# Performance work log

Measured on AMD Instinct MI355X. Metric: run time of the kernel, lower is better.

## Reference

```python
import jax, jax.numpy as jnp
import numpy as np

N_TOKENS = 8192
TOP_K = 2
N_EXPERTS = 8
D_IN = 2048
D_OUT = 2048


def setup_inputs() -> dict:
    key = jax.random.key(0)
    k1, k2, k3, k4 = jax.random.split(key, 4)
    inputs = jax.random.normal(k1, (N_TOKENS, D_IN), dtype=jnp.float32)
    # stored as [E, out, in], matching nn.Parameter(torch.empty(E, output_size, input_size))
    expert_weights = 0.02 * jax.random.normal(k2, (N_EXPERTS, D_OUT, D_IN), dtype=jnp.float32)
    gates = jax.nn.softmax(jax.random.normal(k3, (N_TOKENS, TOP_K), dtype=jnp.float32), axis=-1)
    # per (token, slot) expert assignment, then sort by expert as the router would
    flat_experts = jax.random.randint(k4, (N_TOKENS * TOP_K,), 0, N_EXPERTS, dtype=jnp.int32)
    sorted_scattered_idxs = jnp.argsort(flat_experts).astype(jnp.int32)
    sorted_expert_idxs = flat_experts[sorted_scattered_idxs]
    expert_offsets = jnp.cumsum(jnp.bincount(flat_experts, length=N_EXPERTS)).astype(jnp.int32)
    return {
        "inputs": inputs,
        "expert_weights": expert_weights,
        "gates": gates,
        "k": TOP_K,
        "sorted_expert_idxs": sorted_expert_idxs,
        "sorted_scattered_idxs": sorted_scattered_idxs,
        "expert_offsets": expert_offsets,
    }


def reference(inputs, expert_weights, gates, k, sorted_expert_idxs, sorted_scattered_idxs, expert_offsets):
    N, d_in = inputs.shape
    E = expert_weights.shape[0]
    Nk = N * k
    # forward permutes weight [E, out, in] -> [E, in, out]
    W = jnp.transpose(expert_weights, (0, 2, 1))
    d_out = W.shape[-1]
    # invert the sort: expert id for each flat (token, slot) index
    expert_per_flat = jnp.zeros((Nk,), dtype=sorted_expert_idxs.dtype).at[
        sorted_scattered_idxs].set(sorted_expert_idxs)
    # scatter2scatter: out_flat[j] = x[j // k] @ W[expert_per_flat[j]]
    x_rep = jnp.repeat(inputs, k, axis=0)  # [N*k, d_in]
    out_flat = jnp.zeros((Nk, d_out), dtype=inputs.dtype)
    for e in range(E):  # small fixed expert count; masked grouped GEMM
        mask = (expert_per_flat == e)[:, None]
        out_flat = out_flat + jnp.where(mask, x_rep, 0.0) @ W[e]
    # combine: (gates.unsqueeze(1) @ output_expanded).squeeze(1)
    out = jnp.einsum('nk,nkd->nd', gates, out_flat.reshape(N, k, d_out))
    return out
```

## Files before the change

kernel.cpp:

```cpp
#include <hip/hip_runtime.h>
#include <hip/hip_bf16.h>
#include <stdint.h>

#define NTOK   8192
#define TOPK   2
#define NEXP   8
#define DIN    2048
#define DOUT   2048
#define NK     (NTOK*TOPK)

#define BM 256
#define BN 128
#define BK 32
#define KTILES  (DIN/BK)
#define SLOT    24576
#define NBUF    3

typedef __bf16 bf16_8 __attribute__((ext_vector_type(8)));
typedef float  f32x4  __attribute__((ext_vector_type(4)));

__device__ __forceinline__ void gl2lds16(const void* g, void* l) {
  auto gp = reinterpret_cast<const __attribute__((address_space(1))) uint32_t*>(
      reinterpret_cast<uintptr_t>(g));
  auto lp = reinterpret_cast<__attribute__((address_space(3))) uint32_t*>(
      reinterpret_cast<uintptr_t>(l));
  __builtin_amdgcn_global_load_lds(gp, lp, 16, 0, 0);
}

__global__ void cvt_all(const float4* __restrict__ w, uint4* __restrict__ wD,
                        const float4* __restrict__ x, uint4* __restrict__ xD,
                        int nW) {
  int b = blockIdx.x;
  const float4* src;
  uint4* dst;
  int i;
  if (b < nW) { src = w; dst = wD; i = b * 256 + threadIdx.x; }
  else        { src = x; dst = xD; i = (b - nW) * 256 + threadIdx.x; }
  float4 a0 = src[2 * i];
  float4 a1 = src[2 * i + 1];
  union { __bf16 h[8]; uint4 u; } r;
  r.h[0] = (__bf16)a0.x; r.h[1] = (__bf16)a0.y; r.h[2] = (__bf16)a0.z; r.h[3] = (__bf16)a0.w;
  r.h[4] = (__bf16)a1.x; r.h[5] = (__bf16)a1.y; r.h[6] = (__bf16)a1.z; r.h[7] = (__bf16)a1.w;
  dst[i] = r.u;
}

__global__ __launch_bounds__(512, 4)
void moe_gemm(const __bf16* __restrict__ X,
              const __bf16* __restrict__ W,
              const int* __restrict__ ssi,
              const int* __restrict__ offs,
              __bf16* __restrict__ flat)
{
  __shared__ char lds[NBUF * SLOT];
  __shared__ int  sTok[BM];
  __shared__ int  sF[BM];

  const int tid = threadIdx.x;
  const int bid = blockIdx.x;
  const int nt  = bid & 15;
  const int mtg = bid >> 4;

  int start = 0, end = 0, e, cum = 0, prev = 0, mloc = 0, found = 0;
  for (e = 0; e < NEXP; ++e) {
    int oe  = offs[e];
    int seg = oe - prev;
    int t   = (seg + BM - 1) >> 8;
    if (mtg < cum + t) { start = prev; end = oe; mloc = mtg - cum; found = 1; break; }
    cum += t; prev = oe;
  }
  if (!found) return;

  const int m0 = start + mloc * BM;

  if (tid < BM) {
    int p     = m0 + tid;
    int valid = p < end;
    int f     = ssi[valid ? p : (end - 1)];
    sTok[tid] = f >> 1;
    sF[tid]   = valid ? f : -1;
  }
  __syncthreads();

  const int rs = tid >> 2;
  const int kc = (tid & 3) ^ ((tid >> 3) & 3);
  const __bf16* pA0 = X + (size_t)sTok[rs]       * DIN + kc * 8;
  const __bf16* pA1 = X + (size_t)sTok[rs + 128] * DIN + kc * 8;
  const __bf16* wBp = W + (size_t)e * DOUT * DIN + (size_t)(nt * BN) * DIN;
  const __bf16* pB0 = wBp + (size_t)rs * DIN + kc * 8;
  char* wsl = (char*)lds + (tid >> 6) * 1024;

  gl2lds16(pA0, wsl);           gl2lds16(pA1, wsl + 8192);
  gl2lds16(pB0, wsl + 16384);
  pA0 += BK; pA1 += BK; pB0 += BK;
  gl2lds16(pA0, wsl + SLOT);    gl2lds16(pA1, wsl + SLOT + 8192);
  gl2lds16(pB0, wsl + SLOT + 16384);
  pA0 += BK; pA1 += BK; pB0 += BK;

  const int w   = tid >> 6;
  const int l   = tid & 63;
  const int wm  = w >> 1, wn = w & 1;
  const int lr  = l & 15;
  const int kq  = l >> 4;
  const int kqs = kq ^ ((lr >> 1) & 3);
  const char* aBase = (const char*)lds + (wm * 64 + lr) * 64 + kqs * 16;
  const char* bBase = (const char*)lds + 16384 + (wn * 64 + lr) * 64 + kqs * 16;

  asm volatile("s_waitcnt vmcnt(3)" ::: "memory");
  __builtin_amdgcn_s_barrier();

  f32x4 acc[4][4] = {};
  int rOff = 0;
  int sOff = 2 * SLOT;

  for (int t = 0; t < KTILES; ++t) {
    if (t < KTILES - 2) {
      char* d = wsl + sOff;
      gl2lds16(pA0, d);  gl2lds16(pA1, d + 8192);  gl2lds16(pB0, d + 16384);
      pA0 += BK; pA1 += BK; pB0 += BK;
      sOff = (sOff == (NBUF - 1) * SLOT) ? 0 : sOff + SLOT;
    }

    const char* aB = aBase + rOff;
    const char* bB = bBase + rOff;
    rOff = (rOff == (NBUF - 1) * SLOT) ? 0 : rOff + SLOT;

    bf16_8 af[4], bf[4];
#pragma unroll
    for (int i = 0; i < 4; ++i) af[i] = *(const bf16_8*)(aB + i * 1024);
#pragma unroll
    for (int i = 0; i < 4; ++i) bf[i] = *(const bf16_8*)(bB + i * 1024);

#pragma unroll
    for (int am = 0; am < 4; ++am)
#pragma unroll
      for (int bn = 0; bn < 4; ++bn)
        acc[am][bn] = __builtin_amdgcn_mfma_f32_16x16x32_bf16(
            af[am], bf[bn], acc[am][bn], 0, 0, 0);

    if (t < KTILES - 2)       { asm volatile("s_waitcnt vmcnt(3)" ::: "memory"); }
    else if (t == KTILES - 2) { asm volatile("s_waitcnt vmcnt(0)" ::: "memory"); }
    if (t < KTILES - 1) __builtin_amdgcn_s_barrier();
  }

  const int colBase = nt * BN + wn * 64 + lr;
  const int rq = kq * 4;
#pragma unroll
  for (int am = 0; am < 4; ++am) {
#pragma unroll
    for (int v = 0; v < 4; ++v) {
      int rl = wm * 64 + am * 16 + rq + v;
      int f  = sF[rl];
      if (f < 0) continue;
      __bf16* row = flat + (size_t)f * DOUT + colBase;
#pragma unroll
      for (int bn = 0; bn < 4; ++bn)
        row[bn * 16] = (__bf16)acc[am][bn][v];
    }
  }
}

__global__ __launch_bounds__(256)
void combine(const __bf16* __restrict__ flat, const float* __restrict__ gates,
             float* __restrict__ out) {
  const int n = blockIdx.x;
  const int c = threadIdx.x * 8;
  bf16_8 y0 = *(const bf16_8*)(flat + (size_t)(2 * n)     * DOUT + c);
  bf16_8 y1 = *(const bf16_8*)(flat + (size_t)(2 * n + 1) * DOUT + c);
  const float2 g = *(const float2*)(gates + 2 * n);
  float o[8];
#pragma unroll
  for (int j = 0; j < 8; ++j)
    o[j] = g.x * (float)y0[j] + g.y * (float)y1[j];
  float4* dst = (float4*)(out + (size_t)n * DOUT + c);
  dst[0] = *(float4*)&o[0];
  dst[1] = *(float4*)&o[4];
}

extern "C" void kernel_launch(void* const* d_in, const int* in_sizes, int n_in,
                              void* d_out, int out_size, void* d_ws, size_t ws_size,
                              hipStream_t stream) {
  const float* inputs = (const float*)d_in[0];
  const float* ew     = (const float*)d_in[1];
  const float* gates  = (const float*)d_in[2];
  const int*   ssi    = (const int*)d_in[5];
  const int*   offs   = (const int*)d_in[6];
  float* out = (float*)d_out;

  __bf16* wsW = (__bf16*)d_ws;
  __bf16* wsX = wsW + (size_t)NEXP * DOUT * DIN;
  __bf16* wsF = wsX + (size_t)NTOK * DIN;

  const int n8w = NEXP * DOUT * DIN / 8;
  const int n8x = NTOK * DIN / 8;
  const int nWb = n8w / 256, nXb = n8x / 256;
  cvt_all<<<nWb + nXb, 256, 0, stream>>>((const float4*)ew, (uint4*)wsW,
                                         (const float4*)inputs, (uint4*)wsX, nWb);

  moe_gemm<<<72 * 16, 512, 0, stream>>>(wsX, wsW, ssi, offs, wsF);
  combine<<<NTOK, 256, 0, stream>>>(wsF, gates, out);
}
```

Measured before the change: 437.0 us.

## Fuse gate combine into GEMM epilogue via atomics and remap block order

Drops the separate combine kernel and the bf16 intermediate buffer. The GEMM epilogue now scales each accumulator by its gate and atomically adds it into the float output, which is zeroed first with a memset. The block index is also permuted across groups of eight, presumably to spread work across XCDs or improve cache locality. The cost is scattered fp32 atomic adds with 4-byte strided writes in place of plain stores, and an extra memset of the output.

```diff
diff --git a/kernel.cpp b/kernel.cpp
--- a/kernel.cpp
+++ b/kernel.cpp
@@ -49,14 +49,17 @@
               const __bf16* __restrict__ W,
               const int* __restrict__ ssi,
               const int* __restrict__ offs,
-              __bf16* __restrict__ flat)
+              const float* __restrict__ gates,
+              float* __restrict__ out)
 {
   __shared__ char lds[NBUF * SLOT];
   __shared__ int  sTok[BM];
   __shared__ int  sF[BM];
 
   const int tid = threadIdx.x;
-  const int bid = blockIdx.x;
+  const int nwg = gridDim.x;
+  const int b0  = blockIdx.x;
+  const int bid = (b0 & 7) * (nwg >> 3) + (b0 >> 3);
   const int nt  = bid & 15;
   const int mtg = bid >> 4;
 
@@ -151,29 +154,13 @@
       int rl = wm * 64 + am * 16 + rq + v;
       int f  = sF[rl];
       if (f < 0) continue;
-      __bf16* row = flat + (size_t)f * DOUT + colBase;
+      float g = gates[f];
+      float* row = out + (size_t)(f >> 1) * DOUT + colBase;
 #pragma unroll
       for (int bn = 0; bn < 4; ++bn)
-        row[bn * 16] = (__bf16)acc[am][bn][v];
+        unsafeAtomicAdd(&row[bn * 16], g * acc[am][bn][v]);
     }
   }
-}
-
-__global__ __launch_bounds__(256)
-void combine(const __bf16* __restrict__ flat, const float* __restrict__ gates,
-             float* __restrict__ out) {
-  const int n = blockIdx.x;
-  const int c = threadIdx.x * 8;
-  bf16_8 y0 = *(const bf16_8*)(flat + (size_t)(2 * n)     * DOUT + c);
-  bf16_8 y1 = *(const bf16_8*)(flat + (size_t)(2 * n + 1) * DOUT + c);
-  const float2 g = *(const float2*)(gates + 2 * n);
-  float o[8];
-#pragma unroll
-  for (int j = 0; j < 8; ++j)
-    o[j] = g.x * (float)y0[j] + g.y * (float)y1[j];
-  float4* dst = (float4*)(out + (size_t)n * DOUT + c);
-  dst[0] = *(float4*)&o[0];
-  dst[1] = *(float4*)&o[4];
 }
 
 extern "C" void kernel_launch(void* const* d_in, const int* in_sizes, int n_in,
@@ -188,7 +175,8 @@
 
   __bf16* wsW = (__bf16*)d_ws;
   __bf16* wsX = wsW + (size_t)NEXP * DOUT * DIN;
-  __bf16* wsF = wsX + (size_t)NTOK * DIN;
+
+  hipMemsetAsync(out, 0, (size_t)NTOK * DOUT * sizeof(float), stream);
 
   const int n8w = NEXP * DOUT * DIN / 8;
   const int n8x = NTOK * DIN / 8;
@@ -196,6 +184,5 @@
   cvt_all<<<nWb + nXb, 256, 0, stream>>>((const float4*)ew, (uint4*)wsW,
                                          (const float4*)inputs, (uint4*)wsX, nWb);
 
-  moe_gemm<<<72 * 16, 512, 0, stream>>>(wsX, wsW, ssi, offs, wsF);
-  combine<<<NTOK, 256, 0, stream>>>(wsF, gates, out);
+  moe_gemm<<<72 * 16, 512, 0, stream>>>(wsX, wsW, ssi, offs, gates, out);
 }
```

Result: slower. 478.1 us (+9.4%).

## Switch MoE GEMM to 32x32x16 MFMA tiles and remap block order

Applied to the files above, without the earlier changes.

The inner loop now uses 32x32x16 bf16 MFMA with 2x2 accumulator tiles per wave instead of 16x16x32 with 4x4 tiles. This roughly halves the LDS fragment reads per MFMA flop and uses fewer, larger matrix instructions. The LDS read addressing and epilogue row/column mapping are rewritten for the new MFMA layout. Block indices are also permuted across groups of eight, likely to spread neighbouring tiles across XCDs for L2 locality, at the cost of extra index arithmetic.

```diff
diff --git a/kernel.cpp b/kernel.cpp
--- a/kernel.cpp
+++ b/kernel.cpp
@@ -17,7 +17,7 @@
 #define NBUF    3
 
 typedef __bf16 bf16_8 __attribute__((ext_vector_type(8)));
-typedef float  f32x4  __attribute__((ext_vector_type(4)));
+typedef float  f32x16 __attribute__((ext_vector_type(16)));
 
 __device__ __forceinline__ void gl2lds16(const void* g, void* l) {
   auto gp = reinterpret_cast<const __attribute__((address_space(1))) uint32_t*>(
@@ -56,7 +56,9 @@
   __shared__ int  sF[BM];
 
   const int tid = threadIdx.x;
-  const int bid = blockIdx.x;
+  const int nwg = gridDim.x;
+  const int b0  = blockIdx.x;
+  const int bid = (b0 & 7) * (nwg >> 3) + (b0 >> 3);
   const int nt  = bid & 15;
   const int mtg = bid >> 4;
 
@@ -99,16 +101,18 @@
   const int w   = tid >> 6;
   const int l   = tid & 63;
   const int wm  = w >> 1, wn = w & 1;
-  const int lr  = l & 15;
-  const int kq  = l >> 4;
-  const int kqs = kq ^ ((lr >> 1) & 3);
-  const char* aBase = (const char*)lds + (wm * 64 + lr) * 64 + kqs * 16;
-  const char* bBase = (const char*)lds + 16384 + (wn * 64 + lr) * 64 + kqs * 16;
+  const int r32 = l & 31;
+  const int h   = l >> 5;
+  const int s   = (r32 >> 1) & 3;
+  const int co0 = ((2 * 0 + h) ^ s) * 16;
+  const int co1 = ((2 * 1 + h) ^ s) * 16;
+  const char* aBase = (const char*)lds + (wm * 64 + r32) * 64;
+  const char* bBase = (const char*)lds + 16384 + (wn * 64 + r32) * 64;
 
   asm volatile("s_waitcnt vmcnt(3)" ::: "memory");
   __builtin_amdgcn_s_barrier();
 
-  f32x4 acc[4][4] = {};
+  f32x16 acc[2][2] = {};
   int rOff = 0;
   int sOff = 2 * SLOT;
 
@@ -124,37 +128,46 @@
     const char* bB = bBase + rOff;
     rOff = (rOff == (NBUF - 1) * SLOT) ? 0 : rOff + SLOT;
 
-    bf16_8 af[4], bf[4];
-#pragma unroll
-    for (int i = 0; i < 4; ++i) af[i] = *(const bf16_8*)(aB + i * 1024);
-#pragma unroll
-    for (int i = 0; i < 4; ++i) bf[i] = *(const bf16_8*)(bB + i * 1024);
-
-#pragma unroll
-    for (int am = 0; am < 4; ++am)
-#pragma unroll
-      for (int bn = 0; bn < 4; ++bn)
-        acc[am][bn] = __builtin_amdgcn_mfma_f32_16x16x32_bf16(
-            af[am], bf[bn], acc[am][bn], 0, 0, 0);
+    bf16_8 a0[2], a1[2], bb0[2], bb1[2];
+#pragma unroll
+    for (int mi = 0; mi < 2; ++mi) {
+      a0[mi] = *(const bf16_8*)(aB + mi * 2048 + co0);
+      a1[mi] = *(const bf16_8*)(aB + mi * 2048 + co1);
+    }
+#pragma unroll
+    for (int ni = 0; ni < 2; ++ni) {
+      bb0[ni] = *(const bf16_8*)(bB + ni * 2048 + co0);
+      bb1[ni] = *(const bf16_8*)(bB + ni * 2048 + co1);
+    }
+
+#pragma unroll
+    for (int mi = 0; mi < 2; ++mi)
+#pragma unroll
+      for (int ni = 0; ni < 2; ++ni) {
+        acc[mi][ni] = __builtin_amdgcn_mfma_f32_32x32x16_bf16(
+            a0[mi], bb0[ni], acc[mi][ni], 0, 0, 0);
+        acc[mi][ni] = __builtin_amdgcn_mfma_f32_32x32x16_bf16(
+            a1[mi], bb1[ni], acc[mi][ni], 0, 0, 0);
+      }
 
     if (t < KTILES - 2)       { asm volatile("s_waitcnt vmcnt(3)" ::: "memory"); }
     else if (t == KTILES - 2) { asm volatile("s_waitcnt vmcnt(0)" ::: "memory"); }
     if (t < KTILES - 1) __builtin_amdgcn_s_barrier();
   }
 
-  const int colBase = nt * BN + wn * 64 + lr;
-  const int rq = kq * 4;
-#pragma unroll
-  for (int am = 0; am < 4; ++am) {
-#pragma unroll
-    for (int v = 0; v < 4; ++v) {
-      int rl = wm * 64 + am * 16 + rq + v;
+  const int colBase = nt * BN + wn * 64 + r32;
+#pragma unroll
+  for (int mi = 0; mi < 2; ++mi) {
+#pragma unroll
+    for (int reg = 0; reg < 16; ++reg) {
+      int q  = reg >> 2, v = reg & 3;
+      int rl = wm * 64 + mi * 32 + q * 8 + v + h * 4;
       int f  = sF[rl];
       if (f < 0) continue;
       __bf16* row = flat + (size_t)f * DOUT + colBase;
 #pragma unroll
-      for (int bn = 0; bn < 4; ++bn)
-        row[bn * 16] = (__bf16)acc[am][bn][v];
+      for (int ni = 0; ni < 2; ++ni)
+        row[ni * 32] = (__bf16)acc[mi][ni][reg];
     }
   }
 }
```

Measured after the change: 444.6 us. No clear change (+1.7%).
